# Kernel optimization log

Hardware: AMD Instinct MI355X
Metric: run time of the kernel (lower is better)

## Reference

```python
import jax, jax.numpy as jnp
import numpy as np

NUM_HEADS = 16
HIDDEN = 1024
HEAD_DIM = HIDDEN // NUM_HEADS
B, L = 1, 2048


def setup_inputs() -> dict:
    key = jax.random.key(0)
    ks = jax.random.split(key, 5)
    scale = 1.0 / np.sqrt(HIDDEN)
    x = jax.random.normal(ks[0], (B, L, HIDDEN), dtype=jnp.float32)
    Wq = jax.random.normal(ks[1], (HIDDEN, HIDDEN), dtype=jnp.float32) * scale
    Wk = jax.random.normal(ks[2], (HIDDEN, HIDDEN), dtype=jnp.float32) * scale
    Wv = jax.random.normal(ks[3], (HIDDEN, HIDDEN), dtype=jnp.float32) * scale
    Wo = jax.random.normal(ks[4], (HIDDEN, HIDDEN), dtype=jnp.float32) * scale
    return {"x": x, "Wq": Wq, "Wk": Wk, "Wv": Wv, "Wo": Wo}


def reference(x, Wq, Wk, Wv, Wo):
    Bx, Lx, _ = x.shape
    # nn.Linear computes x @ W.T (bias=False)
    q = (x @ Wq.T).reshape(Bx, Lx, NUM_HEADS, HEAD_DIM)
    k = (x @ Wk.T).reshape(Bx, Lx, NUM_HEADS, HEAD_DIM)
    v = (x @ Wv.T).reshape(Bx, Lx, NUM_HEADS, HEAD_DIM)
    # elu(.)+1 feature map
    q = jax.nn.elu(q) + 1.0
    k = jax.nn.elu(k) + 1.0
    # causal linear-attention state via cumsum of kv outer products
    kv = jnp.einsum('blhd,blhe->blhde', k, v)           # [B,L,H,D,D]
    kv_cumsum = jnp.cumsum(kv, axis=1)
    k_cumsum = jnp.cumsum(k, axis=1)
    out = jnp.einsum('blhd,blhde->blhe', q, kv_cumsum)   # [B,L,H,D]
    denom = jnp.clip(jnp.einsum('blhd,blhd->blh', q, k_cumsum), 1e-6, None)
    out = out / denom[..., None]
    return out.reshape(Bx, Lx, HIDDEN) @ Wo.T
```

## Files before the change

kernel.cpp:

```cpp
#include <hip/hip_runtime.h>
#include <hip/hip_bf16.h>

typedef __attribute__((ext_vector_type(8))) short short8;
typedef __attribute__((ext_vector_type(4))) float floatx4;
typedef __attribute__((ext_vector_type(8))) unsigned short ushortx8;
typedef __attribute__((ext_vector_type(4))) unsigned short ushortx4;
typedef unsigned short u16;

#define HIDDEN 1024
#define NH 16
#define HD 64
#define SEQ 2048
#define CHUNK 128
#define NCHUNK (SEQ / CHUNK)

__device__ __forceinline__ u16 f2bf(float f) {
    union { float f; unsigned u; } v; v.f = f;
    unsigned r = v.u + 0x7fffu + ((v.u >> 16) & 1u);
    return (u16)(r >> 16);
}
__device__ __forceinline__ float bf2f(u16 u) {
    union { unsigned u; float f; } v; v.u = ((unsigned)u) << 16;
    return v.f;
}

__device__ __forceinline__ void gl_lds16(const u16* g, u16* l) {
    __builtin_amdgcn_global_load_lds(
        (const __attribute__((address_space(1))) void*)g,
        (__attribute__((address_space(3))) void*)l,
        16, 0, 0);
}

__global__ __launch_bounds__(256)
void convert_all(const float* __restrict__ x,  const float* __restrict__ Wq,
                 const float* __restrict__ Wk, const float* __restrict__ Wv,
                 const float* __restrict__ Wo,
                 u16* __restrict__ xb, u16* __restrict__ Wb, u16* __restrict__ Wob)
{
    const int total4 = 1572864;
    for (int idx = blockIdx.x * 256 + threadIdx.x; idx < total4; idx += gridDim.x * 256) {
        const float4* src; u16* dst; int off;
        if (idx < 524288)       { src = (const float4*)x;  dst = xb;            off = idx; }
        else if (idx < 786432)  { src = (const float4*)Wq; dst = Wb;            off = idx - 524288; }
        else if (idx < 1048576) { src = (const float4*)Wk; dst = Wb + 1048576;  off = idx - 786432; }
        else if (idx < 1310720) { src = (const float4*)Wv; dst = Wb + 2097152;  off = idx - 1048576; }
        else                    { src = (const float4*)Wo; dst = Wob;           off = idx - 1310720; }
        float4 v = src[off];
        ushortx4 u = { f2bf(v.x), f2bf(v.y), f2bf(v.z), f2bf(v.w) };
        *(ushortx4*)(dst + (size_t)off * 4) = u;
    }
}

__global__ __launch_bounds__(256, 3)
void qkv_gemm64(const u16* __restrict__ A, const u16* __restrict__ Bm,
                u16* __restrict__ qkb, u16* __restrict__ kT_b, u16* __restrict__ vT_b)
{
    __shared__ u16 As[64 * 64];
    __shared__ u16 Bs[128 * 64];
    const int n0 = blockIdx.x * 128, m0 = blockIdx.y * 64;
    const int t = threadIdx.x;
    const int lane = t & 63, wave = t >> 6;
    const int ln = lane & 15, q4 = lane >> 4;
    const int wm = (wave >> 1) * 32, wn = (wave & 1) * 64;
    const int r_in = t >> 3;
    const int csw = (((t & 7) ^ (r_in & 7)) << 3);

    const u16* Ag = A + (size_t)(m0 + r_in) * 1024 + csw;
    const u16* Bg = Bm + (size_t)(n0 + r_in) * 1024 + csw;

    floatx4 acc[2][4];
#pragma unroll
    for (int i = 0; i < 2; i++)
#pragma unroll
        for (int j = 0; j < 4; j++) acc[i][j] = (floatx4)0.0f;

    for (int k0 = 0; k0 < 1024; k0 += 64) {
        if (k0) __syncthreads();
        gl_lds16(Ag, &As[t * 8]);
        gl_lds16(Ag + 32 * 1024, &As[2048 + t * 8]);
#pragma unroll
        for (int i = 0; i < 4; i++)
            gl_lds16(Bg + (size_t)i * 32 * 1024, &Bs[i * 2048 + t * 8]);
        Ag += 64; Bg += 64;
        __syncthreads();
#pragma unroll
        for (int s = 0; s < 2; s++) {
            const int rc = (((s * 4 + q4) ^ (ln & 7)) << 3);
            short8 af[2], bfr[4];
#pragma unroll
            for (int i = 0; i < 2; i++)
                af[i] = *(const short8*)&As[(wm + i * 16 + ln) * 64 + rc];
#pragma unroll
            for (int j = 0; j < 4; j++)
                bfr[j] = *(const short8*)&Bs[(wn + j * 16 + ln) * 64 + rc];
#pragma unroll
            for (int i = 0; i < 2; i++)
#pragma unroll
                for (int j = 0; j < 4; j++)
                    acc[i][j] = __builtin_amdgcn_mfma_f32_16x16x32_bf16(af[i], bfr[j], acc[i][j], 0, 0, 0);
        }
    }
    const int grp = n0 >> 10;
#pragma unroll
    for (int i = 0; i < 2; i++)
#pragma unroll
        for (int j = 0; j < 4; j++) {
            const int mb = m0 + wm + i * 16 + q4 * 4;
            const int n = n0 + wn + j * 16 + ln;
            const int nh = n & 1023, h = nh >> 6, e = nh & 63;
            float vals[4];
#pragma unroll
            for (int r = 0; r < 4; r++) {
                float v = acc[i][j][r];
                if (grp < 2) v = (v > 0.f) ? (v + 1.f) : __expf(v);
                vals[r] = v;
            }
            if (grp == 0) {
#pragma unroll
                for (int r = 0; r < 4; r++) qkb[(size_t)(mb + r) * 2048 + nh] = f2bf(vals[r]);
            } else if (grp == 1) {
#pragma unroll
                for (int r = 0; r < 4; r++) qkb[(size_t)(mb + r) * 2048 + 1024 + nh] = f2bf(vals[r]);
                ushortx4 u = { f2bf(vals[0]), f2bf(vals[1]), f2bf(vals[2]), f2bf(vals[3]) };
                *(ushortx4*)&kT_b[(size_t)(h * 64 + e) * 2048 + mb] = u;
            } else {
                ushortx4 u = { f2bf(vals[0]), f2bf(vals[1]), f2bf(vals[2]), f2bf(vals[3]) };
                *(ushortx4*)&vT_b[(size_t)(h * 64 + e) * 2048 + mb] = u;
            }
        }
}

__global__ __launch_bounds__(256, 2)
void chunk_stats2(const u16* __restrict__ kT_b, const u16* __restrict__ vT_b,
                  float* __restrict__ S_ws, float* __restrict__ ksum_ws)
{
    __shared__ u16 kT_l[64 * 128];
    __shared__ u16 vT_l[64 * 128];
    const int c = blockIdx.x, h = blockIdx.y;
    const int t = threadIdx.x;
    const int lane = t & 63, w = t >> 6;
    const int ln = lane & 15, q4 = lane >> 4;
#pragma unroll
    for (int i = 0; i < 4; i++) {
        const int d0 = w * 16 + i * 4 + (lane >> 4);
        const int cc = lane & 15;
        const size_t gsrc = (size_t)(h * 64 + d0) * 2048 + c * 128 + ((cc ^ (d0 & 7)) << 3);
        gl_lds16(kT_b + gsrc, &kT_l[(w * 16 + i * 4) * 128 + lane * 8]);
        gl_lds16(vT_b + gsrc, &vT_l[(w * 16 + i * 4) * 128 + lane * 8]);
    }
    __syncthreads();
    floatx4 sacc[4];
#pragma unroll
    for (int j = 0; j < 4; j++) sacc[j] = (floatx4)0.0f;
#pragma unroll
    for (int ks = 0; ks < 4; ks++) {
        const int rc = (((ks * 4 + q4) ^ (ln & 7)) << 3);
        short8 af = *(const short8*)&kT_l[(w * 16 + ln) * 128 + rc];
#pragma unroll
        for (int j = 0; j < 4; j++) {
            short8 bfr = *(const short8*)&vT_l[(j * 16 + ln) * 128 + rc];
            sacc[j] = __builtin_amdgcn_mfma_f32_16x16x32_bf16(af, bfr, sacc[j], 0, 0, 0);
        }
    }
    float* Sp = S_ws + ((size_t)(h * NCHUNK + c) << 12);
#pragma unroll
    for (int j = 0; j < 4; j++)
#pragma unroll
        for (int r = 0; r < 4; r++) {
            int d = w * 16 + q4 * 4 + r;
            int e = j * 16 + ln;
            Sp[e * 64 + d] = sacc[j][r];
        }
    if (t < 64) {
        float s = 0.f;
#pragma unroll
        for (int cc = 0; cc < 16; cc++) {
            ushortx8 v8 = *(const ushortx8*)&kT_l[t * 128 + cc * 8];
#pragma unroll
            for (int jj = 0; jj < 8; jj++) s += bf2f(v8[jj]);
        }
        ksum_ws[(h * NCHUNK + c) * 64 + t] = s;
    }
}

__global__ __launch_bounds__(256, 1)
void attn_out2(const u16* __restrict__ qkb, const u16* __restrict__ vT_b,
               const float* __restrict__ S_ws, const float* __restrict__ ksum_ws,
               u16* __restrict__ attnb)
{
    __shared__ __align__(16) u16 smem[29824];
    u16* q_l   = smem;
    u16* k_l   = smem + 8192;
    u16* kvT_l = smem + 16384;
    u16* P_l   = smem;
    u16* vT_l  = smem + 20992;
    float* kpref  = (float*)(smem + 29184);
    float* denom2 = kpref + 64;

    const int c = blockIdx.x, h = blockIdx.y;
    const int t = threadIdx.x;
    const int lane = t & 63, w = t >> 6;
    const int ln = lane & 15, q4 = lane >> 4;

#pragma unroll
    for (int i = 0; i < 4; i++) {
        const int l = i * 32 + w * 8 + (lane >> 3);
        const int cc = lane & 7;
        const size_t gq = (size_t)(c * CHUNK + l) * 2048 + h * 64 + ((cc ^ (l & 7)) << 3);
        gl_lds16(qkb + gq,        &q_l[(i * 32 + w * 8) * 64 + lane * 8]);
        gl_lds16(qkb + gq + 1024, &k_l[(i * 32 + w * 8) * 64 + lane * 8]);
        const int d0 = w * 16 + i * 4 + (lane >> 4);
        const int cv = lane & 15;
        gl_lds16(vT_b + (size_t)(h * 64 + d0) * 2048 + c * 128 + ((cv ^ (d0 & 7)) << 3),
                 &vT_l[(w * 16 + i * 4) * 128 + lane * 8]);
    }
    {
        const int e = t >> 2, db = (t & 3) * 16;
        float kv[16];
#pragma unroll
        for (int i = 0; i < 16; i++) kv[i] = 0.f;
        for (int cp = 0; cp < c; cp++) {
            const float* Sp = S_ws + ((size_t)(h * NCHUNK + cp) << 12) + e * 64 + db;
#pragma unroll
            for (int g = 0; g < 4; g++) {
                float4 s4 = *(const float4*)(Sp + g * 4);
                kv[g * 4 + 0] += s4.x; kv[g * 4 + 1] += s4.y;
                kv[g * 4 + 2] += s4.z; kv[g * 4 + 3] += s4.w;
            }
        }
#pragma unroll
        for (int g = 0; g < 4; g++) {
            ushortx4 u = { f2bf(kv[g * 4 + 0]), f2bf(kv[g * 4 + 1]),
                           f2bf(kv[g * 4 + 2]), f2bf(kv[g * 4 + 3]) };
            *(ushortx4*)&kvT_l[e * 72 + db + g * 4] = u;
        }
        if (t < 64) {
            float s = 0.f;
            for (int cp = 0; cp < c; cp++) s += ksum_ws[(h * NCHUNK + cp) * 64 + t];
            kpref[t] = s;
        }
    }
    __syncthreads();

    const int pm = (w >> 1) * 64, pn = (w & 1) * 64;
    floatx4 pacc[4][4];
#pragma unroll
    for (int i = 0; i < 4; i++)
#pragma unroll
        for (int j = 0; j < 4; j++) pacc[i][j] = (floatx4)0.0f;
#pragma unroll
    for (int s = 0; s < 2; s++) {
        const int rc = (((s * 4 + q4) ^ (ln & 7)) << 3);
        short8 af[4], bfr[4];
#pragma unroll
        for (int i = 0; i < 4; i++)
            af[i] = *(const short8*)&q_l[(pm + i * 16 + ln) * 64 + rc];
#pragma unroll
        for (int j = 0; j < 4; j++)
            bfr[j] = *(const short8*)&k_l[(pn + j * 16 + ln) * 64 + rc];
#pragma unroll
        for (int i = 0; i < 4; i++)
#pragma unroll
            for (int j = 0; j < 4; j++)
                pacc[i][j] = __builtin_amdgcn_mfma_f32_16x16x32_bf16(af[i], bfr[j], pacc[i][j], 0, 0, 0);
    }
#pragma unroll
    for (int i = 0; i < 4; i++)
#pragma unroll
        for (int r = 0; r < 4; r++) {
            int rowi = pm + i * 16 + q4 * 4 + r;
            float rs = 0.f;
#pragma unroll
            for (int j = 0; j < 4; j++) {
                int col = pn + j * 16 + ln;
                float p = pacc[i][j][r];
                if (col > rowi) p = 0.f;
                pacc[i][j][r] = p;
                rs += p;
            }
#pragma unroll
            for (int off = 1; off < 16; off <<= 1) rs += __shfl_xor(rs, off, 64);
            if (ln == 0) denom2[(w & 1) * 128 + rowi] = rs;
        }
    const int ob = w * 32;
    floatx4 oacc[2][4];
#pragma unroll
    for (int i = 0; i < 2; i++)
#pragma unroll
        for (int j = 0; j < 4; j++) oacc[i][j] = (floatx4)0.0f;
#pragma unroll
    for (int s = 0; s < 2; s++) {
        const int rc = (((s * 4 + q4) ^ (ln & 7)) << 3);
        short8 af[2], bfr[4];
#pragma unroll
        for (int i2 = 0; i2 < 2; i2++)
            af[i2] = *(const short8*)&q_l[(ob + i2 * 16 + ln) * 64 + rc];
#pragma unroll
        for (int j = 0; j < 4; j++)
            bfr[j] = *(const short8*)&kvT_l[(j * 16 + ln) * 72 + s * 32 + q4 * 8];
#pragma unroll
        for (int i2 = 0; i2 < 2; i2++)
#pragma unroll
            for (int j = 0; j < 4; j++)
                oacc[i2][j] = __builtin_amdgcn_mfma_f32_16x16x32_bf16(af[i2], bfr[j], oacc[i2][j], 0, 0, 0);
    }
    __syncthreads();
    if (t < 128) {
        float s = 0.f;
#pragma unroll
        for (int c8 = 0; c8 < 8; c8++) {
            ushortx8 v8 = *(const ushortx8*)&q_l[t * 64 + ((c8 ^ (t & 7)) << 3)];
#pragma unroll
            for (int jj = 0; jj < 8; jj++) s += bf2f(v8[jj]) * kpref[c8 * 8 + jj];
        }
        denom2[t] += s;
    }
    __syncthreads();
#pragma unroll
    for (int i = 0; i < 4; i++)
#pragma unroll
        for (int j = 0; j < 4; j++)
#pragma unroll
            for (int r = 0; r < 4; r++) {
                int rowi = pm + i * 16 + q4 * 4 + r;
                int col = pn + j * 16 + ln;
                P_l[rowi * 136 + col] = f2bf(pacc[i][j][r]);
            }
    __syncthreads();
    for (int ks = 0; ks <= w; ks++) {
        short8 af[2], bfr[4];
#pragma unroll
        for (int i2 = 0; i2 < 2; i2++)
            af[i2] = *(const short8*)&P_l[(ob + i2 * 16 + ln) * 136 + ks * 32 + q4 * 8];
        const int rc = (((ks * 4 + q4) ^ (ln & 7)) << 3);
#pragma unroll
        for (int j = 0; j < 4; j++)
            bfr[j] = *(const short8*)&vT_l[(j * 16 + ln) * 128 + rc];
#pragma unroll
        for (int i2 = 0; i2 < 2; i2++)
#pragma unroll
            for (int j = 0; j < 4; j++)
                oacc[i2][j] = __builtin_amdgcn_mfma_f32_16x16x32_bf16(af[i2], bfr[j], oacc[i2][j], 0, 0, 0);
    }
#pragma unroll
    for (int i2 = 0; i2 < 2; i2++)
#pragma unroll
        for (int j = 0; j < 4; j++)
#pragma unroll
            for (int r = 0; r < 4; r++) {
                int rowi = ob + i2 * 16 + q4 * 4 + r;
                int e = j * 16 + ln;
                float den = denom2[rowi] + denom2[128 + rowi];
                den = fmaxf(den, 1e-6f);
                float val = oacc[i2][j][r] / den;
                attnb[(size_t)(c * CHUNK + rowi) * HIDDEN + h * HD + e] = f2bf(val);
            }
}

__global__ __launch_bounds__(256, 3)
void out_gemm64(const u16* __restrict__ A, const u16* __restrict__ Bm,
                float* __restrict__ out)
{
    __shared__ u16 As[64 * 64];
    __shared__ u16 Bs[64 * 64];
    const int n0 = blockIdx.x * 64, m0 = blockIdx.y * 64;
    const int t = threadIdx.x;
    const int lane = t & 63, wave = t >> 6;
    const int ln = lane & 15, q4 = lane >> 4;
    const int wm = (wave >> 1) * 32, wn = (wave & 1) * 32;
    const int r_in = t >> 3;
    const int csw = (((t & 7) ^ (r_in & 7)) << 3);

    const u16* Ag = A + (size_t)(m0 + r_in) * 1024 + csw;
    const u16* Bg = Bm + (size_t)(n0 + r_in) * 1024 + csw;

    floatx4 acc[2][2];
#pragma unroll
    for (int i = 0; i < 2; i++)
#pragma unroll
        for (int j = 0; j < 2; j++) acc[i][j] = (floatx4)0.0f;

    for (int k0 = 0; k0 < 1024; k0 += 64) {
        if (k0) __syncthreads();
        gl_lds16(Ag, &As[t * 8]);
        gl_lds16(Ag + 32 * 1024, &As[2048 + t * 8]);
        gl_lds16(Bg, &Bs[t * 8]);
        gl_lds16(Bg + 32 * 1024, &Bs[2048 + t * 8]);
        Ag += 64; Bg += 64;
        __syncthreads();
#pragma unroll
        for (int s = 0; s < 2; s++) {
            const int rc = (((s * 4 + q4) ^ (ln & 7)) << 3);
            short8 af[2], bfr[2];
#pragma unroll
            for (int i = 0; i < 2; i++)
                af[i] = *(const short8*)&As[(wm + i * 16 + ln) * 64 + rc];
#pragma unroll
            for (int j = 0; j < 2; j++)
                bfr[j] = *(const short8*)&Bs[(wn + j * 16 + ln) * 64 + rc];
#pragma unroll
            for (int i = 0; i < 2; i++)
#pragma unroll
                for (int j = 0; j < 2; j++)
                    acc[i][j] = __builtin_amdgcn_mfma_f32_16x16x32_bf16(af[i], bfr[j], acc[i][j], 0, 0, 0);
        }
    }
#pragma unroll
    for (int i = 0; i < 2; i++)
#pragma unroll
        for (int j = 0; j < 2; j++)
#pragma unroll
            for (int r = 0; r < 4; r++) {
                int m = m0 + wm + i * 16 + q4 * 4 + r;
                int n = n0 + wn + j * 16 + ln;
                out[(size_t)m * 1024 + n] = acc[i][j][r];
            }
}

extern "C" void kernel_launch(void* const* d_in, const int* in_sizes, int n_in,
                              void* d_out, int out_size, void* d_ws, size_t ws_size,
                              hipStream_t stream)
{
    const float* x  = (const float*)d_in[0];
    const float* Wq = (const float*)d_in[1];
    const float* Wk = (const float*)d_in[2];
    const float* Wv = (const float*)d_in[3];
    const float* Wo = (const float*)d_in[4];
    float* out = (float*)d_out;

    char* ws = (char*)d_ws;
    const size_t MB = 1024 * 1024;
    u16* xb    = (u16*)(ws);
    u16* Wb    = (u16*)(ws + 4 * MB);
    u16* Wob   = (u16*)(ws + 10 * MB);
    u16* qkb   = (u16*)(ws + 12 * MB);
    u16* kT_b  = (u16*)(ws + 20 * MB);
    u16* vT_b  = (u16*)(ws + 24 * MB);
    float* S_ws    = (float*)(ws + 28 * MB);
    float* ksum_ws = (float*)(ws + 32 * MB);
    u16* attnb = (u16*)(ws + 33 * MB);

    convert_all<<<2048, 256, 0, stream>>>(x, Wq, Wk, Wv, Wo, xb, Wb, Wob);
    qkv_gemm64<<<dim3(24, 32), 256, 0, stream>>>(xb, Wb, qkb, kT_b, vT_b);
    chunk_stats2<<<dim3(NCHUNK, NH), 256, 0, stream>>>(kT_b, vT_b, S_ws, ksum_ws);
    attn_out2<<<dim3(NCHUNK, NH), 256, 0, stream>>>(qkb, vT_b, S_ws, ksum_ws, attnb);
    out_gemm64<<<dim3(16, 32), 256, 0, stream>>>(attnb, Wob, out);
}
```

Measured before the change: 130.1 us.

## Fuse chunk-state computation into attention kernel, recomputing prefix KV via MFMA

Removes the separate chunk_stats kernel and the fp32 S/ksum workspace round trip. Each attention block now recomputes the prefix KV state by looping over all previous chunks with MFMA, accumulating in registers, and gets the k-sum through an MFMA with an all-ones operand. The P tile in LDS switches from a padded layout to an XOR swizzle. This saves one launch and global traffic but adds redundant quadratic work that is unevenly spread, since later chunks loop over more prefix chunks.

Result: no change. 132.3 us (+1.8%).

```diff
diff --git a/kernel.cpp b/kernel.cpp
--- a/kernel.cpp
+++ b/kernel.cpp
@@ -7,12 +7,10 @@
 typedef __attribute__((ext_vector_type(4))) unsigned short ushortx4;
 typedef unsigned short u16;
 
-#define HIDDEN 1024
 #define NH 16
-#define HD 64
 #define SEQ 2048
 #define CHUNK 128
-#define NCHUNK (SEQ / CHUNK)
+#define NCHUNK 16
 
 __device__ __forceinline__ u16 f2bf(float f) {
     union { float f; unsigned u; } v; v.f = f;
@@ -23,7 +21,6 @@
     union { unsigned u; float f; } v; v.u = ((unsigned)u) << 16;
     return v.f;
 }
-
 __device__ __forceinline__ void gl_lds16(const u16* g, u16* l) {
     __builtin_amdgcn_global_load_lds(
         (const __attribute__((address_space(1))) void*)g,
@@ -130,77 +127,57 @@
         }
 }
 
-__global__ __launch_bounds__(256, 2)
-void chunk_stats2(const u16* __restrict__ kT_b, const u16* __restrict__ vT_b,
-                  float* __restrict__ S_ws, float* __restrict__ ksum_ws)
+__global__ __launch_bounds__(256, 1)
+void attn_fused(const u16* __restrict__ qkb, const u16* __restrict__ kT_b,
+                const u16* __restrict__ vT_b, u16* __restrict__ attnb)
 {
-    __shared__ u16 kT_l[64 * 128];
-    __shared__ u16 vT_l[64 * 128];
+    __shared__ __align__(16) u16 smem[29824];
+    u16* kT_s  = smem;
+    u16* vT_s  = smem + 8192;
+    u16* vT_l  = smem;
+    u16* q_l   = smem + 8192;
+    u16* k_l   = smem + 16384;
+    u16* P_l   = smem + 8192;
+    u16* kvT_l = smem + 24576;
+    float* kpref  = (float*)(smem + 29184);
+    float* denom2 = (float*)(smem + 29312);
+
     const int c = blockIdx.x, h = blockIdx.y;
     const int t = threadIdx.x;
     const int lane = t & 63, w = t >> 6;
     const int ln = lane & 15, q4 = lane >> 4;
-#pragma unroll
-    for (int i = 0; i < 4; i++) {
-        const int d0 = w * 16 + i * 4 + (lane >> 4);
-        const int cc = lane & 15;
-        const size_t gsrc = (size_t)(h * 64 + d0) * 2048 + c * 128 + ((cc ^ (d0 & 7)) << 3);
-        gl_lds16(kT_b + gsrc, &kT_l[(w * 16 + i * 4) * 128 + lane * 8]);
-        gl_lds16(vT_b + gsrc, &vT_l[(w * 16 + i * 4) * 128 + lane * 8]);
+
+    floatx4 sacc[4];
+    floatx4 sksum = (floatx4)0.0f;
+#pragma unroll
+    for (int j = 0; j < 4; j++) sacc[j] = (floatx4)0.0f;
+    const short one_bf = (short)0x3F80;
+    const short8 a_ones = { one_bf, one_bf, one_bf, one_bf,
+                            one_bf, one_bf, one_bf, one_bf };
+    for (int cp = 0; cp < c; cp++) {
+        __syncthreads();
+#pragma unroll
+        for (int i = 0; i < 4; i++) {
+            const int d0 = w * 16 + i * 4 + (lane >> 4);
+            const int cc = lane & 15;
+            const size_t gsrc = (size_t)(h * 64 + d0) * 2048 + cp * 128 + ((cc ^ (d0 & 7)) << 3);
+            gl_lds16(kT_b + gsrc, &kT_s[(w * 16 + i * 4) * 128 + lane * 8]);
+            gl_lds16(vT_b + gsrc, &vT_s[(w * 16 + i * 4) * 128 + lane * 8]);
+        }
+        __syncthreads();
+#pragma unroll
+        for (int ks = 0; ks < 4; ks++) {
+            const int rc = (((ks * 4 + q4) ^ (ln & 7)) << 3);
+            short8 af = *(const short8*)&kT_s[(w * 16 + ln) * 128 + rc];
+            sksum = __builtin_amdgcn_mfma_f32_16x16x32_bf16(a_ones, af, sksum, 0, 0, 0);
+#pragma unroll
+            for (int j = 0; j < 4; j++) {
+                short8 bfr = *(const short8*)&vT_s[(j * 16 + ln) * 128 + rc];
+                sacc[j] = __builtin_amdgcn_mfma_f32_16x16x32_bf16(af, bfr, sacc[j], 0, 0, 0);
+            }
+        }
     }
     __syncthreads();
-    floatx4 sacc[4];
-#pragma unroll
-    for (int j = 0; j < 4; j++) sacc[j] = (floatx4)0.0f;
-#pragma unroll
-    for (int ks = 0; ks < 4; ks++) {
-        const int rc = (((ks * 4 + q4) ^ (ln & 7)) << 3);
-        short8 af = *(const short8*)&kT_l[(w * 16 + ln) * 128 + rc];
-#pragma unroll
-        for (int j = 0; j < 4; j++) {
-            short8 bfr = *(const short8*)&vT_l[(j * 16 + ln) * 128 + rc];
-            sacc[j] = __builtin_amdgcn_mfma_f32_16x16x32_bf16(af, bfr, sacc[j], 0, 0, 0);
-        }
-    }
-    float* Sp = S_ws + ((size_t)(h * NCHUNK + c) << 12);
-#pragma unroll
-    for (int j = 0; j < 4; j++)
-#pragma unroll
-        for (int r = 0; r < 4; r++) {
-            int d = w * 16 + q4 * 4 + r;
-            int e = j * 16 + ln;
-            Sp[e * 64 + d] = sacc[j][r];
-        }
-    if (t < 64) {
-        float s = 0.f;
-#pragma unroll
-        for (int cc = 0; cc < 16; cc++) {
-            ushortx8 v8 = *(const ushortx8*)&kT_l[t * 128 + cc * 8];
-#pragma unroll
-            for (int jj = 0; jj < 8; jj++) s += bf2f(v8[jj]);
-        }
-        ksum_ws[(h * NCHUNK + c) * 64 + t] = s;
-    }
-}
-
-__global__ __launch_bounds__(256, 1)
-void attn_out2(const u16* __restrict__ qkb, const u16* __restrict__ vT_b,
-               const float* __restrict__ S_ws, const float* __restrict__ ksum_ws,
-               u16* __restrict__ attnb)
-{
-    __shared__ __align__(16) u16 smem[29824];
-    u16* q_l   = smem;
-    u16* k_l   = smem + 8192;
-    u16* kvT_l = smem + 16384;
-    u16* P_l   = smem;
-    u16* vT_l  = smem + 20992;
-    float* kpref  = (float*)(smem + 29184);
-    float* denom2 = kpref + 64;
-
-    const int c = blockIdx.x, h = blockIdx.y;
-    const int t = threadIdx.x;
-    const int lane = t & 63, w = t >> 6;
-    const int ln = lane & 15, q4 = lane >> 4;
 
 #pragma unroll
     for (int i = 0; i < 4; i++) {
@@ -214,32 +191,13 @@
         gl_lds16(vT_b + (size_t)(h * 64 + d0) * 2048 + c * 128 + ((cv ^ (d0 & 7)) << 3),
                  &vT_l[(w * 16 + i * 4) * 128 + lane * 8]);
     }
-    {
-        const int e = t >> 2, db = (t & 3) * 16;
-        float kv[16];
-#pragma unroll
-        for (int i = 0; i < 16; i++) kv[i] = 0.f;
-        for (int cp = 0; cp < c; cp++) {
-            const float* Sp = S_ws + ((size_t)(h * NCHUNK + cp) << 12) + e * 64 + db;
-#pragma unroll
-            for (int g = 0; g < 4; g++) {
-                float4 s4 = *(const float4*)(Sp + g * 4);
-                kv[g * 4 + 0] += s4.x; kv[g * 4 + 1] += s4.y;
-                kv[g * 4 + 2] += s4.z; kv[g * 4 + 3] += s4.w;
-            }
-        }
-#pragma unroll
-        for (int g = 0; g < 4; g++) {
-            ushortx4 u = { f2bf(kv[g * 4 + 0]), f2bf(kv[g * 4 + 1]),
-                           f2bf(kv[g * 4 + 2]), f2bf(kv[g * 4 + 3]) };
-            *(ushortx4*)&kvT_l[e * 72 + db + g * 4] = u;
-        }
-        if (t < 64) {
-            float s = 0.f;
-            for (int cp = 0; cp < c; cp++) s += ksum_ws[(h * NCHUNK + cp) * 64 + t];
-            kpref[t] = s;
-        }
-    }
+#pragma unroll
+    for (int j = 0; j < 4; j++) {
+        const int e = j * 16 + ln;
+        ushortx4 u = { f2bf(sacc[j][0]), f2bf(sacc[j][1]), f2bf(sacc[j][2]), f2bf(sacc[j][3]) };
+        *(ushortx4*)&kvT_l[e * 72 + w * 16 + q4 * 4] = u;
+    }
+    if (q4 == 0) kpref[w * 16 + ln] = sksum[0];
     __syncthreads();
 
     const int pm = (w >> 1) * 64, pn = (w & 1) * 64;
@@ -324,14 +282,16 @@
             for (int r = 0; r < 4; r++) {
                 int rowi = pm + i * 16 + q4 * 4 + r;
                 int col = pn + j * 16 + ln;
-                P_l[rowi * 136 + col] = f2bf(pacc[i][j][r]);
+                P_l[rowi * 128 + (col ^ ((rowi & 7) << 3))] = f2bf(pacc[i][j][r]);
             }
     __syncthreads();
     for (int ks = 0; ks <= w; ks++) {
         short8 af[2], bfr[4];
 #pragma unroll
-        for (int i2 = 0; i2 < 2; i2++)
-            af[i2] = *(const short8*)&P_l[(ob + i2 * 16 + ln) * 136 + ks * 32 + q4 * 8];
+        for (int i2 = 0; i2 < 2; i2++) {
+            const int row = ob + i2 * 16 + ln;
+            af[i2] = *(const short8*)&P_l[row * 128 + ((((ks * 4 + q4) ^ (row & 7))) << 3)];
+        }
         const int rc = (((ks * 4 + q4) ^ (ln & 7)) << 3);
 #pragma unroll
         for (int j = 0; j < 4; j++)
@@ -353,7 +313,7 @@
                 float den = denom2[rowi] + denom2[128 + rowi];
                 den = fmaxf(den, 1e-6f);
                 float val = oacc[i2][j][r] / den;
-                attnb[(size_t)(c * CHUNK + rowi) * HIDDEN + h * HD + e] = f2bf(val);
+                attnb[(size_t)(c * CHUNK + rowi) * 1024 + h * 64 + e] = f2bf(val);
             }
 }
 
@@ -436,13 +396,10 @@
     u16* qkb   = (u16*)(ws + 12 * MB);
     u16* kT_b  = (u16*)(ws + 20 * MB);
     u16* vT_b  = (u16*)(ws + 24 * MB);
-    float* S_ws    = (float*)(ws + 28 * MB);
-    float* ksum_ws = (float*)(ws + 32 * MB);
-    u16* attnb = (u16*)(ws + 33 * MB);
+    u16* attnb = (u16*)(ws + 28 * MB);
 
     convert_all<<<2048, 256, 0, stream>>>(x, Wq, Wk, Wv, Wo, xb, Wb, Wob);
     qkv_gemm64<<<dim3(24, 32), 256, 0, stream>>>(xb, Wb, qkb, kT_b, vT_b);
-    chunk_stats2<<<dim3(NCHUNK, NH), 256, 0, stream>>>(kT_b, vT_b, S_ws, ksum_ws);
-    attn_out2<<<dim3(NCHUNK, NH), 256, 0, stream>>>(qkb, vT_b, S_ws, ksum_ws, attnb);
+    attn_fused<<<dim3(NCHUNK, NH), 256, 0, stream>>>(qkb, kT_b, vT_b, attnb);
     out_gemm64<<<dim3(16, 32), 256, 0, stream>>>(attnb, Wob, out);
 }
```
